# Kernel tuning notes

Hardware: AMD Instinct MI355X
Metric: run time of the kernel (lower is better)

The kernel has to match this reference:

```python
import jax, jax.numpy as jnp
import numpy as np

BS, H, W = 2, 24, 24
WIDTH = 20
M1 = M2 = 12
N = H * W
NPAIR = N * (N - 1) // 2
COLL_COEF = 0.9  # training=True path (eval path zeroes the collision term entirely)
_IU, _JU = np.triu_indices(N, k=1)  # static pair indices


def _gelu(x):
    return jax.nn.gelu(x, approximate=False)  # torch F.gelu default = exact erf


def _spectral(x, wr, wi):
    # x: (bs, c, h, w); wr/wi: (2, c, c, M1, M2) -> weights1, weights2
    bs, c, h, w = x.shape
    xft = jnp.fft.rfft2(x)  # (bs, c, h, w//2+1) complex64
    w1 = wr[0] + 1j * wi[0]
    w2 = wr[1] + 1j * wi[1]
    top = jnp.einsum('bixy,ioxy->boxy', xft[:, :, :M1, :M2], w1)
    bot = jnp.einsum('bixy,ioxy->boxy', xft[:, :, -M1:, :M2], w2)
    out = jnp.zeros((bs, c, h, w // 2 + 1), dtype=xft.dtype)
    out = out.at[:, :, :M1, :M2].set(top).at[:, :, -M1:, :M2].set(bot)
    return jnp.fft.irfft2(out, s=(h, w))


def _pair_norm(d):
    # d: (bs, c, n, n) -> (bs, n, n); eps keeps grad finite on the zero diagonal
    return jnp.sqrt(jnp.sum(d * d, axis=1) + 1e-12)


def _kinet_dsmc(p, a, vec):
    # p plays the role of x-positions; v = a*dt (dt=1) exactly as in the torch code
    bs, c, h, w = p.shape
    n = h * w
    x = p.reshape(bs, c, n)
    v = a.reshape(bs, c, n)  # v = a * dt
    x_r = _pair_norm(x[:, :, :, None] - x[:, :, None, :])       # (bs, n, n)
    v_r = _pair_norm(v[:, :, :, None] - v[:, :, None, :])       # (bs, n, n)
    v_cm = (v[:, :, :, None] + v[:, :, None, :]) * 0.5          # (bs, c, n, n)
    u_x = jnp.exp(-x_r)
    v_r_max = jnp.max(v_r, axis=(1, 2), keepdims=True)          # (bs, 1, 1)
    mask = v_r / v_r_max * u_x
    cmask = (mask > 1.0 - COLL_COEF).astype(p.dtype)            # (bs, n, n)
    # antisymmetric projection: R[:, :, i, j] = vec_pair for i<j, -vec_pair for i>j, 0 diag
    R = jnp.zeros((bs, c, n, n), p.dtype)
    R = R.at[:, :, _IU, _JU].set(vec).at[:, :, _JU, _IU].set(-vec)
    v_r_leaving = v_r[:, None] * R                               # (bs, c, n, n)
    delta_v = v_cm + v_r_leaving - v[:, :, :, None]
    v_new = v + jnp.sum(delta_v * cmask[:, None], axis=2)
    x_new = x + v_new  # dt = 1
    return x_new.reshape(bs, c, h, w), v_new.reshape(bs, c, h, w)


def _rv_step(rv, ori, s):
    rv = rv * ori + ori + s
    return rv / jnp.linalg.norm(rv, axis=1, keepdims=True)


def _forward(x, v, fc0_w, fc0_b, sc_wr, sc_wi, w_k, w_b, fc1_w, fc1_b, fc2_w, fc2_b, rv_init, rv_s):
    bs, h, w, _ = x.shape
    gx = jnp.broadcast_to(jnp.linspace(0.0, 1.0, h, dtype=x.dtype)[None, :, None, None], (bs, h, w, 1))
    gy = jnp.broadcast_to(jnp.linspace(0.0, 1.0, w, dtype=x.dtype)[None, None, :, None], (bs, h, w, 1))
    x = jnp.concatenate([x, gx, gy], axis=-1)          # (bs, h, w, 12)
    x = x @ fc0_w + fc0_b                              # lift to width
    x = jnp.transpose(x, (0, 3, 1, 2))                 # (bs, width, h, w)
    ori = rv_init / jnp.linalg.norm(rv_init, axis=1, keepdims=True)
    rv = rv_init
    for k in range(4):
        a = _spectral(x, sc_wr[k], sc_wi[k])
        p = jnp.einsum('bchw,oc->bohw', x, w_k[k]) + w_b[k][None, :, None, None]
        rv = _rv_step(rv, ori, rv_s[k])
        x, v = _kinet_dsmc(p, a, rv)
        if k < 3:
            x = _gelu(x)
            v = _gelu(v)
    x = jnp.transpose(x, (0, 2, 3, 1))                 # (bs, h, w, width)
    x = _gelu(x @ fc1_w + fc1_b)
    x = x @ fc2_w + fc2_b
    return x


def setup_inputs() -> dict:
    key = jax.random.key(0)
    ks = jax.random.split(key, 12)
    f = jnp.float32
    scale = 1.0 / (WIDTH * WIDTH)
    xs = -4.0 - 3.0 * jax.random.uniform(ks[9], (4,), f)                 # in [-7, -4]
    signs = jax.random.randint(ks[10], (4,), 0, 2).astype(f) * 2.0 - 1.0
    return {
        'x': jax.random.normal(ks[0], (BS, H, W, 10), f),
        'v': jax.random.normal(ks[1], (BS, WIDTH, H, W), f),
        'fc0_w': jax.random.normal(ks[2], (12, WIDTH), f) * 0.1,
        'fc0_b': jnp.zeros((WIDTH,), f),
        'sc_wr': jax.random.uniform(ks[3], (4, 2, WIDTH, WIDTH, M1, M2), f) * scale,
        'sc_wi': jax.random.uniform(ks[4], (4, 2, WIDTH, WIDTH, M1, M2), f) * scale,
        'w_k': jax.random.normal(ks[5], (4, WIDTH, WIDTH), f) * 0.1,
        'w_b': jnp.zeros((4, WIDTH), f),
        'fc1_w': jax.random.normal(ks[6], (WIDTH, 128), f) * 0.1,
        'fc1_b': jnp.zeros((128,), f),
        'fc2_w': jax.random.normal(ks[7], (128, 1), f) * 0.1,
        'fc2_b': jnp.zeros((1,), f),
        'rv_init': jax.random.normal(ks[8], (BS, WIDTH, NPAIR), f),
        'rv_s': signs * jnp.exp(xs),
    }


def reference(x, v, fc0_w, fc0_b, sc_wr, sc_wi, w_k, w_b, fc1_w, fc1_b, fc2_w, fc2_b, rv_init, rv_s):
    return _forward(x, v, fc0_w, fc0_b, sc_wr, sc_wi, w_k, w_b, fc1_w, fc1_b, fc2_w, fc2_b, rv_init, rv_s)
```

## Files before the change

### kernel.cpp

```cpp
#include <hip/hip_runtime.h>


#define N_     576
#define NPAIR_ 165600
#define C_     20

#define TR_SPEC_B 512
#define TR_INV_B  192
#define TR_PMAX_B 144
#define TRS0 0
#define TRI0 (TR_SPEC_B*288)
#define TRP0 (TRI0 + TR_INV_B*576)

__device__ __forceinline__ float gelu_f(float x){
    return 0.5f * x * (1.0f + erff(x * 0.70710678118654752440f));
}

__device__ __forceinline__ void tr_one(const float* __restrict__ rvi,
                                       float* __restrict__ rvt, int t){
    if (t >= 2*NPAIR_) return;
    int bb = t / NPAIR_, pr = t % NPAIR_;
    size_t ibase = (size_t)bb*C_*NPAIR_ + pr;
    float v[C_];
    #pragma unroll
    for (int c=0;c<C_;c++) v[c] = rvi[ibase + (size_t)c*NPAIR_];
    float4* dst = (float4*)(rvt + (size_t)t*C_);
    #pragma unroll
    for (int q=0;q<5;q++) dst[q] = make_float4(v[4*q],v[4*q+1],v[4*q+2],v[4*q+3]);
}

__device__ __forceinline__ void lift_in(const float* __restrict__ xin, int bb, int hw, float* in){
    int h = hw / 24, wc = hw % 24;
    const float* xp = xin + ((size_t)bb*N_ + hw)*10;
    #pragma unroll
    for (int q=0;q<10;q++) in[q] = xp[q];
    in[10] = (float)h  * (1.0f/23.0f);
    in[11] = (float)wc * (1.0f/23.0f);
}

__global__ void k_specp(const float* __restrict__ x, float* __restrict__ Xr, float* __restrict__ Xi,
                        const float* __restrict__ wk, const float* __restrict__ wb,
                        float* __restrict__ p_t,
                        const float* __restrict__ rvi, float* __restrict__ rvt,
                        const float* __restrict__ xin, const float* __restrict__ fc0w,
                        const float* __restrict__ fc0b, int layer0,
                        unsigned* __restrict__ vmaxu){
    if (blockIdx.x >= 44){
        tr_one(rvi, rvt, TRS0 + (blockIdx.x-44)*288 + (int)threadIdx.x);
        return;
    }
    if (blockIdx.x < 40){
        __shared__ float xt[576], Tr[288], Ti[288], cst[24], snt[24];
        int bc = blockIdx.x;
        int tid = threadIdx.x;
        if (layer0 && bc == 0 && tid < 8) vmaxu[tid] = 0u;
        if (tid < 24){
            float s, c;
            sincosf((float)tid * 0.26179938779914943654f, &s, &c);
            cst[tid]=c; snt[tid]=s;
        }
        if (layer0){
            int bb = bc/20, c = bc%20;
            for (int q=tid;q<576;q+=288){
                float in[12];
                lift_in(xin, bb, q, in);
                float acc = fc0b[c];
                #pragma unroll
                for (int qq=0;qq<12;qq++) acc += in[qq]*fc0w[qq*C_+c];
                xt[q] = acc;
            }
        } else {
            for (int q=tid;q<576;q+=288) xt[q] = x[(size_t)bc*576+q];
        }
        __syncthreads();
        {
            int h = tid/12, ky = tid%12;
            float ar=0.f, ai=0.f;
            for (int w=0;w<24;w++){
                int m = (ky*w) % 24;
                float v = xt[h*24+w];
                ar += v*cst[m];
                ai -= v*snt[m];
            }
            Tr[tid]=ar; Ti[tid]=ai;
        }
        __syncthreads();
        {
            int kx = tid/12, ky = tid%12;
            float ar=0.f, ai=0.f;
            for (int h=0;h<24;h++){
                int m = (kx*h)%24;
                float tr=Tr[h*12+ky], ti=Ti[h*12+ky];
                float cc=cst[m], ss=snt[m];
                ar += tr*cc + ti*ss;
                ai += ti*cc - tr*ss;
            }
            Xr[(size_t)bc*288 + tid] = ar;
            Xi[(size_t)bc*288 + tid] = ai;
        }
    } else {
        __shared__ float swk[400], swb[C_];
        int tid = threadIdx.x;
        for (int q=tid;q<400;q+=288) swk[q]=wk[q];
        if (tid < C_) swb[tid]=wb[tid];
        __syncthreads();
        int t = (blockIdx.x-40)*288 + tid;
        if (t >= 2*N_) return;
        int bb = t / N_, hw = t % N_;
        float xi[C_];
        if (layer0){
            float in[12];
            lift_in(xin, bb, hw, in);
            #pragma unroll
            for (int c=0;c<C_;c++){
                float acc = fc0b[c];
                #pragma unroll
                for (int qq=0;qq<12;qq++) acc += in[qq]*fc0w[qq*C_+c];
                xi[c] = acc;
            }
        } else {
            #pragma unroll
            for (int c=0;c<C_;c++) xi[c] = x[(size_t)(bb*C_+c)*N_+hw];
        }
        float accv[C_];
        #pragma unroll
        for (int o=0;o<C_;o++){
            float acc = swb[o];
            #pragma unroll
            for (int c=0;c<C_;c++) acc += xi[c]*swk[o*C_+c];
            accv[o]=acc;
        }
        float4* dst = (float4*)(p_t + (size_t)t*C_);
        #pragma unroll
        for (int q=0;q<5;q++) dst[q] = make_float4(accv[4*q],accv[4*q+1],accv[4*q+2],accv[4*q+3]);
    }
}

__global__ void k_fft_inv(const float* __restrict__ Xr, const float* __restrict__ Xi,
                          const float* __restrict__ wr, const float* __restrict__ wi,
                          float* __restrict__ a_t,
                          const float* __restrict__ rvi, float* __restrict__ rvt){
    if (blockIdx.x >= 40){
        tr_one(rvi, rvt, TRI0 + (blockIdx.x-40)*576 + (int)threadIdx.x);
        return;
    }
    __shared__ float Fr[288], Fi[288], Yr[288], Yi[288], cst[24], snt[24];
    int bo = blockIdx.x; int bb = bo/20, o = bo%20;
    int tid = threadIdx.x;
    if (tid < 24){
        float s, c;
        sincosf((float)tid * 0.26179938779914943654f, &s, &c);
        cst[tid]=c; snt[tid]=s;
    }
    if (tid < 288){
        int ky = tid%12, kx = tid/12;
        int half = (kx>=12) ? 1 : 0; int mx = kx - half*12;
        float ar=0.f, ai=0.f;
        for (int i=0;i<20;i++){
            float xr = Xr[(size_t)(bb*20+i)*288 + tid];
            float xi = Xi[(size_t)(bb*20+i)*288 + tid];
            size_t widx = ((((size_t)half*20+i)*20+o)*12+mx)*12+ky;
            float wrv = wr[widx], wiv = wi[widx];
            ar += xr*wrv - xi*wiv;
            ai += xr*wiv + xi*wrv;
        }
        Fr[tid]=ar; Fi[tid]=ai;
    }
    __syncthreads();
    if (tid < 288){
        int h = tid/12;
        float ar=0.f, ai=0.f;
        for (int kx=0;kx<24;kx++){
            int m=(kx*h)%24;
            float fr=Fr[kx*12 + (tid%12)], fi=Fi[kx*12 + (tid%12)];
            ar += fr*cst[m] - fi*snt[m];
            ai += fr*snt[m] + fi*cst[m];
        }
        Yr[tid]=ar*(1.0f/24.0f); Yi[tid]=ai*(1.0f/24.0f);
    }
    __syncthreads();
    {
        int h = tid/24, w = tid%24;
        float acc = Yr[h*12+0];
        #pragma unroll
        for (int ky=1;ky<12;ky++){
            int m=(ky*w)%24;
            acc += 2.0f*(Yr[h*12+ky]*cst[m] - Yi[h*12+ky]*snt[m]);
        }
        a_t[((size_t)bb*N_ + tid)*C_ + o] = acc*(1.0f/24.0f);
    }
}

__global__ void k_pairmax(const float* __restrict__ a_t, float* __restrict__ vmax,
                          const float* __restrict__ rvi, float* __restrict__ rvt){
    if (blockIdx.x >= 2*N_){
        tr_one(rvi, rvt, TRP0 + (blockIdx.x-2*N_)*576 + (int)threadIdx.x);
        return;
    }
    __shared__ float ai[C_], wred[9];
    int bb = blockIdx.x/N_, i = blockIdx.x%N_;
    int j = threadIdx.x;
    if (j < C_) ai[j]=a_t[((size_t)bb*N_+i)*C_+j];
    __syncthreads();
    const float4* aj4 = (const float4*)(a_t + ((size_t)bb*N_+j)*C_);
    float ssv=0.f;
    #pragma unroll
    for (int q=0;q<5;q++){
        float4 av = aj4[q];
        float dv;
        dv = ai[4*q+0]-av.x; ssv += dv*dv;
        dv = ai[4*q+1]-av.y; ssv += dv*dv;
        dv = ai[4*q+2]-av.z; ssv += dv*dv;
        dv = ai[4*q+3]-av.w; ssv += dv*dv;
    }
    float m = ssv;
    #pragma unroll
    for (int off=32; off; off>>=1) m = fmaxf(m, __shfl_down(m, off, 64));
    if ((j&63)==0) wred[j>>6] = m;
    __syncthreads();
    if (j==0){
        float mm = wred[0];
        #pragma unroll
        for (int q=1;q<9;q++) mm = fmaxf(mm, wred[q]);
        atomicMax((unsigned int*)&vmax[bb], __float_as_uint(sqrtf(mm+1e-12f)));
    }
}

__global__ void __launch_bounds__(256, 1)
k_vnew(const float* __restrict__ p_t, const float* __restrict__ a_t,
       const float* __restrict__ rvt, const float* __restrict__ vmax,
       const float* __restrict__ rs, int klayer,
       float* __restrict__ xout, int do_head,
       const float* __restrict__ fc1w, const float* __restrict__ fc1b,
       const float* __restrict__ fc2w, const float* __restrict__ fc2b,
       float* __restrict__ out){
    __shared__ float pi[C_], ai[C_];
    __shared__ short hlist[N_];
    __shared__ int cnts[4];
    __shared__ float wacc[4][C_];
    __shared__ float xrow[C_];
    __shared__ float psum[2];
    int bb = blockIdx.x/N_, i = blockIdx.x%N_;
    int tid = threadIdx.x;
    int wid = tid>>6, lane = tid&63;
    if (tid < C_){ pi[tid]=p_t[((size_t)bb*N_+i)*C_+tid]; ai[tid]=a_t[((size_t)bb*N_+i)*C_+tid]; }
    __syncthreads();
    float vm = vmax[bb];
    const float thr = 0.1f;
    const float4* pbase = (const float4*)(p_t + (size_t)bb*N_*C_);
    const float4* abase = (const float4*)(a_t + (size_t)bb*N_*C_);

    int jb = wid*144;
    unsigned long long m0, m1, m2;
    {
        auto test = [&](int j)->bool{
            const float4* pj = pbase + j*5;
            const float4* aj = abase + j*5;
            float ssx=0.f, ssv=0.f;
            #pragma unroll
            for (int q=0;q<5;q++){
                float4 pv = pj[q], av = aj[q];
                float dx, dv;
                dx = pi[4*q+0]-pv.x; dv = ai[4*q+0]-av.x; ssx += dx*dx; ssv += dv*dv;
                dx = pi[4*q+1]-pv.y; dv = ai[4*q+1]-av.y; ssx += dx*dx; ssv += dv*dv;
                dx = pi[4*q+2]-pv.z; dv = ai[4*q+2]-av.z; ssx += dx*dx; ssv += dv*dv;
                dx = pi[4*q+3]-pv.w; dv = ai[4*q+3]-av.w; ssx += dx*dx; ssv += dv*dv;
            }
            float vrv = sqrtf(ssv+1e-12f);
            float uxv = expf(-sqrtf(ssx+1e-12f));
            return ((vrv/vm)*uxv > thr) && (j != i);
        };
        int j = jb + lane;
        m0 = __ballot(test(j));
        m1 = __ballot(test(j+64));
        bool h2 = (lane<16) ? test(jb+128+lane) : false;
        m2 = __ballot(h2);
    }
    if (lane == 0) cnts[wid] = (int)(__popcll(m0)+__popcll(m1)+__popcll(m2));
    __syncthreads();
    int off = 0;
    #pragma unroll
    for (int w=0;w<4;w++) if (w < wid) off += cnts[w];
    int nhit = cnts[0]+cnts[1]+cnts[2]+cnts[3];
    {
        unsigned long long below = (1ULL<<lane)-1ULL;
        int base = off;
        if (m0 & (1ULL<<lane)) hlist[base + __popcll(m0 & below)] = (short)(jb + lane);
        base += (int)__popcll(m0);
        if (m1 & (1ULL<<lane)) hlist[base + __popcll(m1 & below)] = (short)(jb + 64 + lane);
        base += (int)__popcll(m1);
        if (m2 & (1ULL<<lane)) hlist[base + __popcll(m2 & below)] = (short)(jb + 128 + lane);
    }
    __syncthreads();

    float s_arr[4] = { rs[0], rs[1], rs[2], rs[3] };
    float macc[C_];
    #pragma unroll
    for (int c=0;c<C_;c++) macc[c]=0.f;

    for (int t=tid; t<nhit; t+=256){
        int j = hlist[t];
        float av[C_];
        {
            const float4* aj = abase + j*5;
            #pragma unroll
            for (int q=0;q<5;q++){
                float4 aa = aj[q];
                av[4*q+0]=aa.x; av[4*q+1]=aa.y; av[4*q+2]=aa.z; av[4*q+3]=aa.w;
            }
        }
        float ssv=0.f;
        #pragma unroll
        for (int c=0;c<C_;c++){ float dv = ai[c]-av[c]; ssv += dv*dv; }
        float vrij = sqrtf(ssv+1e-12f);
        float sgn = (j<i) ? 1.0f : -1.0f;
        int lo = (j<i)?j:i, hi = (j<i)?i:j;
        int pidx = lo*(2*N_-lo-1)/2 + (hi-lo-1);
        float vrs = sgn*vrij;
        float st[C_];
        {
            const float4* rp = (const float4*)(rvt + ((size_t)bb*NPAIR_ + pidx)*C_);
            #pragma unroll
            for (int q=0;q<5;q++){
                float4 rr = rp[q];
                st[4*q+0]=rr.x; st[4*q+1]=rr.y; st[4*q+2]=rr.z; st[4*q+3]=rr.w;
            }
        }
        float ssq = 0.f;
        #pragma unroll
        for (int c=0;c<C_;c++) ssq += st[c]*st[c];
        float ini = 1.0f/sqrtf(ssq);
        float orc[C_];
        #pragma unroll
        for (int c=0;c<C_;c++) orc[c] = st[c]*ini;
        for (int l=0; l<=klayer; l++){
            float s = s_arr[l];
            float nq = 0.f;
            #pragma unroll
            for (int c=0;c<C_;c++){
                float nv = st[c]*orc[c] + orc[c] + s;
                st[c] = nv; nq += nv*nv;
            }
            float inn = 1.0f/sqrtf(nq);
            #pragma unroll
            for (int c=0;c<C_;c++) st[c] *= inn;
        }
        #pragma unroll
        for (int c=0;c<C_;c++) macc[c] += vrs*st[c] - 0.5f*av[c];
    }
    #pragma unroll
    for (int off2=32; off2; off2>>=1){
        #pragma unroll
        for (int c=0;c<C_;c++) macc[c] += __shfl_xor(macc[c], off2, 64);
    }
    if (lane == 0){
        #pragma unroll
        for (int c=0;c<C_;c++) wacc[wid][c] = macc[c];
    }
    __syncthreads();
    if (!do_head){
        if (tid < C_){
            int c = tid;
            float msum = wacc[0][c]+wacc[1][c]+wacc[2][c]+wacc[3][c];
            float vi = ai[c];
            float vnew = vi + 0.5f*(float)nhit*vi + msum;
            float xn = pi[c] + vnew;
            xout[(size_t)(bb*C_+c)*N_+i] = gelu_f(xn);
        }
    } else {
        if (tid < C_){
            int c = tid;
            float msum = wacc[0][c]+wacc[1][c]+wacc[2][c]+wacc[3][c];
            float vi = ai[c];
            float vnew = vi + 0.5f*(float)nhit*vi + msum;
            xrow[c] = pi[c] + vnew;
        }
        __syncthreads();
        if (tid < 128){
            float h = fc1b[tid];
            #pragma unroll
            for (int c=0;c<C_;c++) h += xrow[c]*fc1w[c*128+tid];
            float g = gelu_f(h)*fc2w[tid];
            #pragma unroll
            for (int off2=32; off2; off2>>=1) g += __shfl_down(g, off2, 64);
            if (lane==0) psum[wid] = g;
        }
        __syncthreads();
        if (tid==0) out[bb*N_+i] = psum[0] + psum[1] + fc2b[0];
    }
}

extern "C" void kernel_launch(void* const* d_in, const int* in_sizes, int n_in,
                              void* d_out, int out_size, void* d_ws, size_t ws_size,
                              hipStream_t stream) {
    const float* in_x   = (const float*)d_in[0];
    const float* fc0_w  = (const float*)d_in[2];
    const float* fc0_b  = (const float*)d_in[3];
    const float* sc_wr  = (const float*)d_in[4];
    const float* sc_wi  = (const float*)d_in[5];
    const float* w_k    = (const float*)d_in[6];
    const float* w_b    = (const float*)d_in[7];
    const float* fc1_w  = (const float*)d_in[8];
    const float* fc1_b  = (const float*)d_in[9];
    const float* fc2_w  = (const float*)d_in[10];
    const float* fc2_b  = (const float*)d_in[11];
    const float* rv_init= (const float*)d_in[12];
    const float* rv_s   = (const float*)d_in[13];
    float* out = (float*)d_out;
    float* ws  = (float*)d_ws;

    float* rvt   = ws;
    float* x_cur = ws + 6624000;
    float* p_t   = ws + 6647040;
    float* a_t   = ws + 6670080;
    float* Xr    = ws + 6693120;
    float* Xi    = ws + 6704640;
    float* vmax  = ws + 6716160;

    for (int k=0;k<4;k++){
        const size_t woff = (size_t)k*115200;
        int g_sp = (k==0) ? 44 + TR_SPEC_B : 44;
        int g_iv = (k==0) ? 40 + TR_INV_B  : 40;
        int g_pm = (k==0) ? 2*N_ + TR_PMAX_B : 2*N_;
        k_specp<<<g_sp, 288, 0, stream>>>(x_cur, Xr, Xi, w_k + k*400, w_b + k*20, p_t,
                                          rv_init, rvt, in_x, fc0_w, fc0_b, (k==0) ? 1 : 0,
                                          (unsigned*)vmax);
        k_fft_inv<<<g_iv, 576, 0, stream>>>(Xr, Xi, sc_wr+woff, sc_wi+woff, a_t, rv_init, rvt);
        k_pairmax<<<g_pm, N_, 0, stream>>>(a_t, vmax + 2*k, rv_init, rvt);
        k_vnew<<<2*N_, 256, 0, stream>>>(p_t, a_t, rvt, vmax + 2*k, rv_s, k,
                                         x_cur, (k==3) ? 1 : 0,
                                         fc1_w, fc1_b, fc2_w, fc2_b, out);
    }
}
```

Before: 209.6 us.

## Fuse forward spectral FFT and inverse spectral conv into one kernel

Merges the forward 2D DFT kernel and the spectral-multiply/inverse-DFT kernel into a single kernel with one block per (batch, output channel). Each block recomputes the forward DFT of all input channels in two groups of ten, staged in shared memory, so the intermediate Xr/Xi global buffers and one launch per layer go away. The cost is redundant forward-transform work across the 20 output-channel blocks and more shared memory per block. The pair-data transpose work is also redistributed over the remaining two kernels.

```diff
diff --git a/kernel.cpp b/kernel.cpp
--- a/kernel.cpp
+++ b/kernel.cpp
@@ -4,13 +4,12 @@
 #define N_     576
 #define NPAIR_ 165600
 #define C_     20
-
-#define TR_SPEC_B 512
-#define TR_INV_B  192
-#define TR_PMAX_B 144
+#define NG     10
+
+#define TR_SCONV_B 431
+#define TR_PMAX_B  144
 #define TRS0 0
-#define TRI0 (TR_SPEC_B*288)
-#define TRP0 (TRI0 + TR_INV_B*576)
+#define TRP0 (TR_SCONV_B*576)
 
 __device__ __forceinline__ float gelu_f(float x){
     return 0.5f * x * (1.0f + erff(x * 0.70710678118654752440f));
@@ -38,73 +37,122 @@
     in[11] = (float)wc * (1.0f/23.0f);
 }
 
-__global__ void k_specp(const float* __restrict__ x, float* __restrict__ Xr, float* __restrict__ Xi,
-                        const float* __restrict__ wk, const float* __restrict__ wb,
-                        float* __restrict__ p_t,
-                        const float* __restrict__ rvi, float* __restrict__ rvt,
-                        const float* __restrict__ xin, const float* __restrict__ fc0w,
-                        const float* __restrict__ fc0b, int layer0,
-                        unsigned* __restrict__ vmaxu){
-    if (blockIdx.x >= 44){
-        tr_one(rvi, rvt, TRS0 + (blockIdx.x-44)*288 + (int)threadIdx.x);
+__global__ void __launch_bounds__(576)
+k_sconv(const float* __restrict__ x, const float* __restrict__ wr, const float* __restrict__ wi,
+        const float* __restrict__ wk, const float* __restrict__ wb,
+        float* __restrict__ p_t, float* __restrict__ a_t,
+        const float* __restrict__ rvi, float* __restrict__ rvt,
+        const float* __restrict__ xin, const float* __restrict__ fc0w,
+        const float* __restrict__ fc0b, int layer0,
+        unsigned* __restrict__ vmaxu){
+    int bid = blockIdx.x;
+    int tid = threadIdx.x;
+    if (bid >= 42){
+        tr_one(rvi, rvt, TRS0 + (bid-42)*576 + tid);
         return;
     }
-    if (blockIdx.x < 40){
-        __shared__ float xt[576], Tr[288], Ti[288], cst[24], snt[24];
-        int bc = blockIdx.x;
-        int tid = threadIdx.x;
-        if (layer0 && bc == 0 && tid < 8) vmaxu[tid] = 0u;
+    if (bid < 40){
+        __shared__ float xg[NG*576];
+        __shared__ float Tr[NG*288], Ti[NG*288];
+        __shared__ float Fr[288], Fi[288], Yr[288], Yi[288];
+        __shared__ float cst[24], snt[24];
+        int bb = bid/20, o = bid%20;
+        if (layer0 && bid == 0 && tid < 8) vmaxu[tid] = 0u;
         if (tid < 24){
             float s, c;
             sincosf((float)tid * 0.26179938779914943654f, &s, &c);
             cst[tid]=c; snt[tid]=s;
         }
-        if (layer0){
-            int bb = bc/20, c = bc%20;
-            for (int q=tid;q<576;q+=288){
-                float in[12];
-                lift_in(xin, bb, q, in);
-                float acc = fc0b[c];
-                #pragma unroll
-                for (int qq=0;qq<12;qq++) acc += in[qq]*fc0w[qq*C_+c];
-                xt[q] = acc;
-            }
-        } else {
-            for (int q=tid;q<576;q+=288) xt[q] = x[(size_t)bc*576+q];
+        float fr = 0.f, fi2 = 0.f;
+        for (int g=0; g<2; ++g){
+            __syncthreads();
+            if (layer0){
+                for (int q=tid; q<NG*576; q+=576){
+                    int cg=q/576, pos=q%576, c=g*NG+cg;
+                    float in[12];
+                    lift_in(xin, bb, pos, in);
+                    float acc = fc0b[c];
+                    #pragma unroll
+                    for (int qq=0;qq<12;qq++) acc += in[qq]*fc0w[qq*C_+c];
+                    xg[q] = acc;
+                }
+            } else {
+                for (int q=tid; q<NG*576; q+=576){
+                    int cg=q/576, pos=q%576, c=g*NG+cg;
+                    xg[q] = x[(size_t)(bb*C_+c)*N_+pos];
+                }
+            }
+            __syncthreads();
+            for (int q=tid; q<NG*288; q+=576){
+                int cg=q/288, r=q%288, h=r/12, ky=r%12;
+                float ar=0.f, ai=0.f;
+                for (int w=0;w<24;w++){
+                    int m = (ky*w) % 24;
+                    float v = xg[cg*576 + h*24+w];
+                    ar += v*cst[m];
+                    ai -= v*snt[m];
+                }
+                Tr[q]=ar; Ti[q]=ai;
+            }
+            __syncthreads();
+            for (int q=tid; q<NG*288; q+=576){
+                int cg=q/288, r=q%288, kx=r/12, ky=r%12;
+                float ar=0.f, ai=0.f;
+                for (int h=0;h<24;h++){
+                    int m = (kx*h)%24;
+                    float tr=Tr[cg*288 + h*12+ky], ti=Ti[cg*288 + h*12+ky];
+                    float cc=cst[m], ss=snt[m];
+                    ar += tr*cc + ti*ss;
+                    ai += ti*cc - tr*ss;
+                }
+                xg[q]        = ar;
+                xg[NG*288+q] = ai;
+            }
+            __syncthreads();
+            if (tid < 288){
+                int ky = tid%12, kx = tid/12;
+                int half = (kx>=12) ? 1 : 0; int mx = kx - half*12;
+                for (int ii=0; ii<NG; ++ii){
+                    int i2 = g*NG + ii;
+                    float xr  = xg[ii*288 + tid];
+                    float xiv = xg[NG*288 + ii*288 + tid];
+                    size_t widx = ((((size_t)half*20+i2)*20+o)*12+mx)*12+ky;
+                    float wrv = wr[widx], wiv = wi[widx];
+                    fr  += xr*wrv - xiv*wiv;
+                    fi2 += xr*wiv + xiv*wrv;
+                }
+            }
+        }
+        if (tid < 288){ Fr[tid]=fr; Fi[tid]=fi2; }
+        __syncthreads();
+        if (tid < 288){
+            int h = tid/12;
+            float ar=0.f, ai=0.f;
+            for (int kx=0;kx<24;kx++){
+                int m=(kx*h)%24;
+                float frv=Fr[kx*12 + (tid%12)], fiv=Fi[kx*12 + (tid%12)];
+                ar += frv*cst[m] - fiv*snt[m];
+                ai += frv*snt[m] + fiv*cst[m];
+            }
+            Yr[tid]=ar*(1.0f/24.0f); Yi[tid]=ai*(1.0f/24.0f);
         }
         __syncthreads();
         {
-            int h = tid/12, ky = tid%12;
-            float ar=0.f, ai=0.f;
-            for (int w=0;w<24;w++){
-                int m = (ky*w) % 24;
-                float v = xt[h*24+w];
-                ar += v*cst[m];
-                ai -= v*snt[m];
-            }
-            Tr[tid]=ar; Ti[tid]=ai;
-        }
-        __syncthreads();
-        {
-            int kx = tid/12, ky = tid%12;
-            float ar=0.f, ai=0.f;
-            for (int h=0;h<24;h++){
-                int m = (kx*h)%24;
-                float tr=Tr[h*12+ky], ti=Ti[h*12+ky];
-                float cc=cst[m], ss=snt[m];
-                ar += tr*cc + ti*ss;
-                ai += ti*cc - tr*ss;
-            }
-            Xr[(size_t)bc*288 + tid] = ar;
-            Xi[(size_t)bc*288 + tid] = ai;
+            int h = tid/24, w = tid%24;
+            float acc = Yr[h*12+0];
+            #pragma unroll
+            for (int ky=1;ky<12;ky++){
+                int m=(ky*w)%24;
+                acc += 2.0f*(Yr[h*12+ky]*cst[m] - Yi[h*12+ky]*snt[m]);
+            }
+            a_t[((size_t)bb*N_ + tid)*C_ + o] = acc*(1.0f/24.0f);
         }
     } else {
         __shared__ float swk[400], swb[C_];
-        int tid = threadIdx.x;
-        for (int q=tid;q<400;q+=288) swk[q]=wk[q];
+        for (int q=tid;q<400;q+=576) swk[q]=wk[q];
         if (tid < C_) swb[tid]=wb[tid];
         __syncthreads();
-        int t = (blockIdx.x-40)*288 + tid;
+        int t = (bid-40)*576 + tid;
         if (t >= 2*N_) return;
         int bb = t / N_, hw = t % N_;
         float xi[C_];
@@ -133,61 +181,6 @@
         float4* dst = (float4*)(p_t + (size_t)t*C_);
         #pragma unroll
         for (int q=0;q<5;q++) dst[q] = make_float4(accv[4*q],accv[4*q+1],accv[4*q+2],accv[4*q+3]);
-    }
-}
-
-__global__ void k_fft_inv(const float* __restrict__ Xr, const float* __restrict__ Xi,
-                          const float* __restrict__ wr, const float* __restrict__ wi,
-                          float* __restrict__ a_t,
-                          const float* __restrict__ rvi, float* __restrict__ rvt){
-    if (blockIdx.x >= 40){
-        tr_one(rvi, rvt, TRI0 + (blockIdx.x-40)*576 + (int)threadIdx.x);
-        return;
-    }
-    __shared__ float Fr[288], Fi[288], Yr[288], Yi[288], cst[24], snt[24];
-    int bo = blockIdx.x; int bb = bo/20, o = bo%20;
-    int tid = threadIdx.x;
-    if (tid < 24){
-        float s, c;
-        sincosf((float)tid * 0.26179938779914943654f, &s, &c);
-        cst[tid]=c; snt[tid]=s;
-    }
-    if (tid < 288){
-        int ky = tid%12, kx = tid/12;
-        int half = (kx>=12) ? 1 : 0; int mx = kx - half*12;
-        float ar=0.f, ai=0.f;
-        for (int i=0;i<20;i++){
-            float xr = Xr[(size_t)(bb*20+i)*288 + tid];
-            float xi = Xi[(size_t)(bb*20+i)*288 + tid];
-            size_t widx = ((((size_t)half*20+i)*20+o)*12+mx)*12+ky;
-            float wrv = wr[widx], wiv = wi[widx];
-            ar += xr*wrv - xi*wiv;
-            ai += xr*wiv + xi*wrv;
-        }
-        Fr[tid]=ar; Fi[tid]=ai;
-    }
-    __syncthreads();
-    if (tid < 288){
-        int h = tid/12;
-        float ar=0.f, ai=0.f;
-        for (int kx=0;kx<24;kx++){
-            int m=(kx*h)%24;
-            float fr=Fr[kx*12 + (tid%12)], fi=Fi[kx*12 + (tid%12)];
-            ar += fr*cst[m] - fi*snt[m];
-            ai += fr*snt[m] + fi*cst[m];
-        }
-        Yr[tid]=ar*(1.0f/24.0f); Yi[tid]=ai*(1.0f/24.0f);
-    }
-    __syncthreads();
-    {
-        int h = tid/24, w = tid%24;
-        float acc = Yr[h*12+0];
-        #pragma unroll
-        for (int ky=1;ky<12;ky++){
-            int m=(ky*w)%24;
-            acc += 2.0f*(Yr[h*12+ky]*cst[m] - Yi[h*12+ky]*snt[m]);
-        }
-        a_t[((size_t)bb*N_ + tid)*C_ + o] = acc*(1.0f/24.0f);
     }
 }
 
@@ -413,19 +406,16 @@
     float* x_cur = ws + 6624000;
     float* p_t   = ws + 6647040;
     float* a_t   = ws + 6670080;
-    float* Xr    = ws + 6693120;
-    float* Xi    = ws + 6704640;
-    float* vmax  = ws + 6716160;
+    float* vmax  = ws + 6693120;
 
     for (int k=0;k<4;k++){
         const size_t woff = (size_t)k*115200;
-        int g_sp = (k==0) ? 44 + TR_SPEC_B : 44;
-        int g_iv = (k==0) ? 40 + TR_INV_B  : 40;
+        int g_sc = (k==0) ? 42 + TR_SCONV_B : 42;
         int g_pm = (k==0) ? 2*N_ + TR_PMAX_B : 2*N_;
-        k_specp<<<g_sp, 288, 0, stream>>>(x_cur, Xr, Xi, w_k + k*400, w_b + k*20, p_t,
-                                          rv_init, rvt, in_x, fc0_w, fc0_b, (k==0) ? 1 : 0,
-                                          (unsigned*)vmax);
-        k_fft_inv<<<g_iv, 576, 0, stream>>>(Xr, Xi, sc_wr+woff, sc_wi+woff, a_t, rv_init, rvt);
+        k_sconv<<<g_sc, 576, 0, stream>>>(x_cur, sc_wr+woff, sc_wi+woff,
+                                          w_k + k*400, w_b + k*20, p_t, a_t,
+                                          rv_init, rvt, in_x, fc0_w, fc0_b,
+                                          (k==0) ? 1 : 0, (unsigned*)vmax);
         k_pairmax<<<g_pm, N_, 0, stream>>>(a_t, vmax + 2*k, rv_init, rvt);
         k_vnew<<<2*N_, 256, 0, stream>>>(p_t, a_t, rvt, vmax + 2*k, rv_s, k,
                                          x_cur, (k==3) ? 1 : 0,
```

Measured after the change: 331.6 us. 1.58x slower.
